# Performance work log

Measured on AMD Instinct MI355X. Metric: run time of the kernel, lower is better.

Reference implementation:

```python
import jax, jax.numpy as jnp
import numpy as np

N_NODES = 50000
N_EDGES = 800000
IN_DIM, HID_DIM, OUT_DIM, N_CLASSES = 128, 256, 64, 40


def _xavier(key, shape):
    fan_in, fan_out = shape[0], shape[1]
    std = float(np.sqrt(2.0 / (fan_in + fan_out)))
    return jax.random.normal(key, shape, dtype=jnp.float32) * std


def gcn_conv(x, W, b, src, dst, n_nodes):
    """PyG GCNConv: add self-loops, symmetric D^-1/2 (A+I) D^-1/2 X W + b."""
    h = x @ W  # [N, out]
    loop = jnp.arange(n_nodes, dtype=src.dtype)
    s = jnp.concatenate([src, loop])  # sources (messages flow src -> dst)
    d = jnp.concatenate([dst, loop])
    ones = jnp.ones(s.shape[0], dtype=h.dtype)
    deg = jax.ops.segment_sum(ones, d, num_segments=n_nodes)  # in-degree incl. self-loop
    dinv = jnp.where(deg > 0, jax.lax.rsqrt(deg), 0.0)
    norm = dinv[s] * dinv[d]  # [E+N]
    msg = h[s] * norm[:, None]
    out = jax.ops.segment_sum(msg, d, num_segments=n_nodes)
    return out + b


def setup_inputs() -> dict:
    key = jax.random.key(0)
    ks = jax.random.split(key, 9)
    x = jax.random.normal(ks[0], (N_NODES, IN_DIM), dtype=jnp.float32)
    edge_index = jax.random.randint(ks[1], (2, N_EDGES), 0, N_NODES, dtype=jnp.int64)
    return {
        "x": x,
        "edge_index": edge_index,
        "W1": _xavier(ks[2], (IN_DIM, HID_DIM)),
        "b1": jnp.zeros((HID_DIM,), jnp.float32),
        "W2": _xavier(ks[3], (HID_DIM, OUT_DIM)),
        "b2": jnp.zeros((OUT_DIM,), jnp.float32),
        "Wp1": _xavier(ks[4], (2 * OUT_DIM, 4 * OUT_DIM)),
        "bp1": jnp.zeros((4 * OUT_DIM,), jnp.float32),
        "Wp2": _xavier(ks[5], (4 * OUT_DIM, OUT_DIM)),
        "bp2": jnp.zeros((OUT_DIM,), jnp.float32),
        "Wc": _xavier(ks[6], (OUT_DIM, N_CLASSES)),
        "bc": jnp.zeros((N_CLASSES,), jnp.float32),
    }


def reference(x, edge_index, W1, b1, W2, b2, Wp1, bp1, Wp2, bp2, Wc, bc):
    src, dst = edge_index[0], edge_index[1]
    n = x.shape[0]
    h = jax.nn.relu(gcn_conv(x, W1, b1, src, dst, n))  # [N, HID]
    f = gcn_conv(h, W2, b2, src, dst, n)  # [N, OUT]
    # edge MLP on gathered endpoint features
    ef = jnp.concatenate([f[src], f[dst]], axis=-1)  # [E, 2*OUT]
    ef = jax.nn.relu(ef @ Wp1 + bp1)  # [E, 4*OUT]
    edge_feats = ef @ Wp2 + bp2  # [E, OUT]
    logits = f @ Wc + bc  # [N, C]
    return f, edge_feats, logits, edge_index
```

## Files before the change

### kernel.cpp

```cpp
#include <hip/hip_runtime.h>

#define N_NODES   50000
#define N_EDGES   800000
#define IN_DIM    128
#define HID_DIM   256
#define OUT_DIM   64
#define N_CLASSES 40

typedef __attribute__((ext_vector_type(8))) short short8;
typedef __attribute__((ext_vector_type(8))) unsigned short ushort8;
typedef __attribute__((ext_vector_type(4))) float f32x4;

__device__ inline short f2bf(float x) {
    unsigned u = __builtin_bit_cast(unsigned, x);
    unsigned r = (u + 0x7FFFu + ((u >> 16) & 1u)) >> 16;
    return (short)r;
}
__device__ inline float bf2f(unsigned short u) {
    unsigned v = ((unsigned)u) << 16;
    return __builtin_bit_cast(float, v);
}
__device__ __host__ inline int swap23(int p) {
    return (p & 0xC3) | ((p >> 2) & 0x0C) | ((p << 2) & 0x30);
}


__global__ void k_prep(const float* __restrict__ x,
                       const float* __restrict__ W1, const float* __restrict__ W2,
                       const float* __restrict__ Wp1, const float* __restrict__ Wp2,
                       unsigned short* __restrict__ xb,
                       short* __restrict__ W1t, short* __restrict__ W2t,
                       short* __restrict__ Wp1t, short* __restrict__ Wp2t,
                       int* __restrict__ degi, int* __restrict__ cursor) {
    int i = blockIdx.x * 256 + threadIdx.x;
    if (i < N_NODES) { degi[i] = 0; cursor[i] = 0; }
    if (i < 128 * 256) {
        int k = i >> 8, n = i & 255;
        W1t[n * 128 + k]  = f2bf(W1[i]);
        Wp1t[n * 128 + k] = f2bf(Wp1[i]);
    }
    if (i < 256 * 64) {
        int p = i >> 6, o = i & 63;
        int h = swap23(p);
        W2t[o * 256 + p]  = f2bf(W2[h * 64 + o]);
        Wp2t[o * 256 + p] = f2bf(Wp2[h * 64 + o]);
    }
    if (i < N_NODES * IN_DIM / 4) {
        float4 v = ((const float4*)x)[i];
        ushort4 u;
        u.x = (unsigned short)f2bf(v.x); u.y = (unsigned short)f2bf(v.y);
        u.z = (unsigned short)f2bf(v.z); u.w = (unsigned short)f2bf(v.w);
        ((ushort4*)xb)[i] = u;
    }
}


__global__ void k_deg_count(const int* __restrict__ dst, int* __restrict__ degi) {
    int e = blockIdx.x * 256 + threadIdx.x;
    if (e < N_EDGES) atomicAdd(&degi[dst[e]], 1);
}

__global__ void k_scan_bsum(const int* __restrict__ vals, int n, int* __restrict__ bsum,
                            float* __restrict__ dinv) {
    __shared__ int sm[256];
    int t = threadIdx.x, i = blockIdx.x * 256 + t;
    int d = (i < n) ? vals[i] : 0;
    if (i < n) dinv[i] = rsqrtf((float)(d + 1));
    sm[t] = d;
    __syncthreads();
    for (int s = 128; s > 0; s >>= 1) {
        if (t < s) sm[t] += sm[t + s];
        __syncthreads();
    }
    if (t == 0) bsum[blockIdx.x] = sm[0];
}

__global__ void k_scan_bscan(int* __restrict__ bsum, int nb) {
    __shared__ int sm[256];
    int t = threadIdx.x;
    int orig = (t < nb) ? bsum[t] : 0;
    sm[t] = orig;
    __syncthreads();
    for (int off = 1; off < 256; off <<= 1) {
        int v = (t >= off) ? sm[t - off] : 0;
        __syncthreads();
        sm[t] += v;
        __syncthreads();
    }
    if (t < nb) bsum[t] = sm[t] - orig;
}

__global__ void k_scan_final(const int* __restrict__ vals, int n,
                             const int* __restrict__ bscan, int* __restrict__ out) {
    __shared__ int sm[256];
    int t = threadIdx.x, i = blockIdx.x * 256 + t;
    int orig = (i < n) ? vals[i] : 0;
    sm[t] = orig;
    __syncthreads();
    for (int off = 1; off < 256; off <<= 1) {
        int v = (t >= off) ? sm[t - off] : 0;
        __syncthreads();
        sm[t] += v;
        __syncthreads();
    }
    int excl = sm[t] - orig + bscan[blockIdx.x];
    if (i < n) out[i] = excl;
    if (i == n - 1) out[n] = excl + orig;
}

__global__ void k_csr_fill(const int* __restrict__ src, const int* __restrict__ dst,
                           const int* __restrict__ csr_off, int* __restrict__ cursor,
                           int* __restrict__ csr_src) {
    int e = blockIdx.x * 256 + threadIdx.x;
    if (e < N_EDGES) {
        int d = dst[e];
        int pos = csr_off[d] + atomicAdd(&cursor[d], 1);
        csr_src[pos] = src[e];
    }
}

__global__ void k_copy_ei(const int* __restrict__ ei, float* __restrict__ out) {
    int j = blockIdx.x * 256 + threadIdx.x;
    if (j < (2 * N_EDGES) / 4) {
        int4 v = ((const int4*)ei)[j];
        float4 o = {(float)v.x, (float)v.y, (float)v.z, (float)v.w};
        ((float4*)out)[j] = o;
    }
}


__global__ __launch_bounds__(256) void k_agg0(const unsigned short* __restrict__ xb,
                                              const float* __restrict__ dinv,
                                              const int* __restrict__ csr_off,
                                              const int* __restrict__ csr_src,
                                              unsigned short* __restrict__ xa) {
    const int v = blockIdx.x * 4 + (threadIdx.x >> 6);
    const int lane = threadIdx.x & 63;
    float dv = dinv[v];
    unsigned c = *(const unsigned*)(xb + (size_t)v * 128 + lane * 2);
    float a0 = bf2f((unsigned short)(c & 0xFFFF)) * dv;
    float a1 = bf2f((unsigned short)(c >> 16)) * dv;
    int beg = csr_off[v], end = csr_off[v + 1];
    for (int base = beg; base < end; base += 64) {
        int idx = base + lane;
        int sj = (idx < end) ? csr_src[idx] : 0;
        float dj = (idx < end) ? dinv[sj] : 0.f;
        int m = min(64, end - base);
        int j = 0;
        for (; j + 4 <= m; j += 4) {
            int s0 = __shfl(sj, j), s1 = __shfl(sj, j + 1);
            int s2 = __shfl(sj, j + 2), s3 = __shfl(sj, j + 3);
            float d0 = __shfl(dj, j), d1 = __shfl(dj, j + 1);
            float d2 = __shfl(dj, j + 2), d3 = __shfl(dj, j + 3);
            unsigned h0 = *(const unsigned*)(xb + (size_t)s0 * 128 + lane * 2);
            unsigned h1 = *(const unsigned*)(xb + (size_t)s1 * 128 + lane * 2);
            unsigned h2 = *(const unsigned*)(xb + (size_t)s2 * 128 + lane * 2);
            unsigned h3 = *(const unsigned*)(xb + (size_t)s3 * 128 + lane * 2);
            a0 += bf2f((unsigned short)(h0 & 0xFFFF)) * d0 + bf2f((unsigned short)(h1 & 0xFFFF)) * d1
                + bf2f((unsigned short)(h2 & 0xFFFF)) * d2 + bf2f((unsigned short)(h3 & 0xFFFF)) * d3;
            a1 += bf2f((unsigned short)(h0 >> 16)) * d0 + bf2f((unsigned short)(h1 >> 16)) * d1
                + bf2f((unsigned short)(h2 >> 16)) * d2 + bf2f((unsigned short)(h3 >> 16)) * d3;
        }
        for (; j < m; j++) {
            int s = __shfl(sj, j);
            float ds = __shfl(dj, j);
            unsigned hv = *(const unsigned*)(xb + (size_t)s * 128 + lane * 2);
            a0 += bf2f((unsigned short)(hv & 0xFFFF)) * ds;
            a1 += bf2f((unsigned short)(hv >> 16)) * ds;
        }
    }
    unsigned o = (unsigned)(unsigned short)f2bf(a0 * dv) |
                 ((unsigned)(unsigned short)f2bf(a1 * dv) << 16);
    *(unsigned*)(xa + (size_t)v * 128 + lane * 2) = o;
}


__global__ __launch_bounds__(256) void k_agg2(const unsigned short* __restrict__ h2b,
                                              const float* __restrict__ dinv,
                                              const int* __restrict__ csr_off,
                                              const int* __restrict__ csr_src,
                                              const float* __restrict__ b2,
                                              const float* __restrict__ Wc,
                                              const float* __restrict__ bc,
                                              float* __restrict__ f_out,
                                              unsigned short* __restrict__ fb,
                                              float* __restrict__ lg_out) {
    const int v = blockIdx.x * 4 + (threadIdx.x >> 6);
    const int lane = threadIdx.x & 63;
    float dv = dinv[v];
    float acc = bf2f(h2b[(size_t)v * 64 + lane]) * dv;
    int beg = csr_off[v], end = csr_off[v + 1];
    for (int base = beg; base < end; base += 64) {
        int idx = base + lane;
        int sj = (idx < end) ? csr_src[idx] : 0;
        float dj = (idx < end) ? dinv[sj] : 0.f;
        int m = min(64, end - base);
        int j = 0;
        for (; j + 4 <= m; j += 4) {
            int s0 = __shfl(sj, j), s1 = __shfl(sj, j + 1);
            int s2 = __shfl(sj, j + 2), s3 = __shfl(sj, j + 3);
            float d0 = __shfl(dj, j), d1 = __shfl(dj, j + 1);
            float d2 = __shfl(dj, j + 2), d3 = __shfl(dj, j + 3);
            float h0 = bf2f(h2b[(size_t)s0 * 64 + lane]);
            float h1 = bf2f(h2b[(size_t)s1 * 64 + lane]);
            float h2 = bf2f(h2b[(size_t)s2 * 64 + lane]);
            float h3 = bf2f(h2b[(size_t)s3 * 64 + lane]);
            acc += h0 * d0 + h1 * d1 + h2 * d2 + h3 * d3;
        }
        for (; j < m; j++) {
            int s = __shfl(sj, j);
            float ds = __shfl(dj, j);
            acc += bf2f(h2b[(size_t)s * 64 + lane]) * ds;
        }
    }
    float r = acc * dv + b2[lane];
    f_out[(size_t)v * 64 + lane] = r;
    fb[(size_t)v * 64 + lane] = (unsigned short)f2bf(r);
    bool act = lane < N_CLASSES;
    float lacc = act ? bc[lane] : 0.f;
    #pragma unroll
    for (int i2 = 0; i2 < 64; i2++) {
        float fi = __shfl(r, i2);
        if (act) lacc += fi * Wc[i2 * N_CLASSES + lane];
    }
    if (act) lg_out[(size_t)v * N_CLASSES + lane] = lacc;
}


__global__ __launch_bounds__(256) void k_gemm1_mfma(const unsigned short* __restrict__ xa,
                                                    const short* __restrict__ W1t,
                                                    const float* __restrict__ b1,
                                                    unsigned short* __restrict__ h1) {
    __shared__ unsigned short xs[64 * 128];
    const int t = threadIdx.x;
    const int lane = t & 63, wv = t >> 6, lr = lane & 15, lg = lane >> 4;
    const int nb = blockIdx.x * 64;

    #pragma unroll
    for (int i = 0; i < 4; i++) {
        int q = t + i * 256, row = q >> 4, seg = q & 15;
        int node = nb + row;
        ushort8 v = {0, 0, 0, 0, 0, 0, 0, 0};
        if (node < N_NODES) v = *(const ushort8*)(xa + (size_t)node * 128 + seg * 8);
        *(ushort8*)((char*)xs + ((row * 256 + seg * 16) ^ ((row & 7) << 4))) = v;
    }

    short8 A1[4][4];
    #pragma unroll
    for (int mi = 0; mi < 4; mi++)
        #pragma unroll
        for (int kt = 0; kt < 4; kt++)
            A1[mi][kt] = *(const short8*)(W1t + (size_t)(wv * 64 + mi * 16 + lr) * 128 + kt * 32 + lg * 8);
    __syncthreads();

    #pragma unroll
    for (int nj = 0; nj < 4; nj++) {
        short8 Bf[4];
        int nr = nj * 16 + lr;
        #pragma unroll
        for (int kt = 0; kt < 4; kt++)
            Bf[kt] = *(const short8*)((const char*)xs + ((nr * 256 + kt * 64 + lg * 16) ^ ((nr & 7) << 4)));
        int node = nb + nr;
        #pragma unroll
        for (int mh = 0; mh < 2; mh++) {
            f32x4 a0 = {0.f, 0.f, 0.f, 0.f}, a1 = {0.f, 0.f, 0.f, 0.f};
            #pragma unroll
            for (int kt = 0; kt < 4; kt++) {
                a0 = __builtin_amdgcn_mfma_f32_16x16x32_bf16(A1[mh * 2 + 0][kt], Bf[kt], a0, 0, 0, 0);
                a1 = __builtin_amdgcn_mfma_f32_16x16x32_bf16(A1[mh * 2 + 1][kt], Bf[kt], a1, 0, 0, 0);
            }
            if (node < N_NODES) {
                float4 b0 = *(const float4*)(b1 + wv * 64 + (mh * 2 + 0) * 16 + lg * 4);
                float4 b1v = *(const float4*)(b1 + wv * 64 + (mh * 2 + 1) * 16 + lg * 4);
                ushort8 pk;
                pk[0] = (unsigned short)f2bf(fmaxf(a0[0] + b0.x, 0.f));
                pk[1] = (unsigned short)f2bf(fmaxf(a0[1] + b0.y, 0.f));
                pk[2] = (unsigned short)f2bf(fmaxf(a0[2] + b0.z, 0.f));
                pk[3] = (unsigned short)f2bf(fmaxf(a0[3] + b0.w, 0.f));
                pk[4] = (unsigned short)f2bf(fmaxf(a1[0] + b1v.x, 0.f));
                pk[5] = (unsigned short)f2bf(fmaxf(a1[1] + b1v.y, 0.f));
                pk[6] = (unsigned short)f2bf(fmaxf(a1[2] + b1v.z, 0.f));
                pk[7] = (unsigned short)f2bf(fmaxf(a1[3] + b1v.w, 0.f));
                *(ushort8*)(h1 + (size_t)node * 256 + wv * 64 + lg * 16 + mh * 8) = pk;
            }
        }
    }
}


__global__ __launch_bounds__(256) void k_gemm2_mfma(const unsigned short* __restrict__ h1,
                                                    const short* __restrict__ W2t,
                                                    unsigned short* __restrict__ h2b) {
    __shared__ unsigned short hs[64 * 256];
    const int t = threadIdx.x;
    const int lane = t & 63, wv = t >> 6, lr = lane & 15, lg = lane >> 4;
    const int nb = blockIdx.x * 64;

    #pragma unroll
    for (int i = 0; i < 8; i++) {
        int q = t + i * 256, row = q >> 5, seg = q & 31;
        int node = nb + row;
        ushort8 v = {0, 0, 0, 0, 0, 0, 0, 0};
        if (node < N_NODES) v = *(const ushort8*)(h1 + (size_t)node * 256 + seg * 8);
        *(ushort8*)((char*)hs + ((row * 512 + seg * 16) ^ ((row & 7) << 4))) = v;
    }

    short8 A2[8];
    #pragma unroll
    for (int kt = 0; kt < 8; kt++)
        A2[kt] = *(const short8*)(W2t + (size_t)(wv * 16 + lr) * 256 + kt * 32 + lg * 8);
    __syncthreads();

    #pragma unroll
    for (int nj = 0; nj < 4; nj++) {
        short8 Bh[8];
        int nr = nj * 16 + lr;
        #pragma unroll
        for (int kt = 0; kt < 8; kt++)
            Bh[kt] = *(const short8*)((const char*)hs + ((nr * 512 + kt * 64 + lg * 16) ^ ((nr & 7) << 4)));
        int node = nb + nr;
        f32x4 acc = {0.f, 0.f, 0.f, 0.f};
        #pragma unroll
        for (int kt = 0; kt < 8; kt++)
            acc = __builtin_amdgcn_mfma_f32_16x16x32_bf16(A2[kt], Bh[kt], acc, 0, 0, 0);
        if (node < N_NODES) {
            ushort4 u;
            u.x = (unsigned short)f2bf(acc[0]); u.y = (unsigned short)f2bf(acc[1]);
            u.z = (unsigned short)f2bf(acc[2]); u.w = (unsigned short)f2bf(acc[3]);
            *(ushort4*)(h2b + (size_t)node * 64 + wv * 16 + lg * 4) = u;
        }
    }
}


__global__ __launch_bounds__(256) void k_egather(const unsigned short* __restrict__ fb,
                                                 const int* __restrict__ src,
                                                 const int* __restrict__ dst,
                                                 char* __restrict__ ef_ws) {
    const int nchunk = N_EDGES * 16;
    for (int q = blockIdx.x * 256 + threadIdx.x; q < nchunk; q += gridDim.x * 256) {
        int e = q >> 4, seg = q & 15;
        int node = (seg < 8) ? src[e] : dst[e];
        ushort8 v = *(const ushort8*)(fb + (size_t)node * 64 + (seg & 7) * 8);
        *(ushort8*)(ef_ws + (size_t)e * 256 + seg * 16) = v;
    }
}


__global__ __launch_bounds__(256) void k_edge_mlpB(
        const char* __restrict__ ef_ws,
        const short* __restrict__ Wp1t, const float* __restrict__ bp1,
        const short* __restrict__ Wp2t, const float* __restrict__ bp2,
        float* __restrict__ out, int n_tiles) {
    __shared__ unsigned short hid_s[2][32 * 256];

    const int t = threadIdx.x;
    const int lane = t & 63, wv = t >> 6, lr = lane & 15, lg = lane >> 4;

    short8 A1[4][4];
    #pragma unroll
    for (int mi = 0; mi < 4; mi++)
        #pragma unroll
        for (int kt = 0; kt < 4; kt++)
            A1[mi][kt] = *(const short8*)(Wp1t + (size_t)(wv * 64 + mi * 16 + lr) * 128 + kt * 32 + lg * 8);
    float4 bb1[4];
    #pragma unroll
    for (int mi = 0; mi < 4; mi++)
        bb1[mi] = *(const float4*)(bp1 + wv * 64 + mi * 16 + lg * 4);
    const float4 bv2 = *(const float4*)(bp2 + wv * 16 + lg * 4);

    int tile = blockIdx.x;
    if (tile >= n_tiles) return;

    short8 Bf[2][4];
    {
        const char* base = ef_ws + (size_t)tile * 8192;
        #pragma unroll
        for (int nj = 0; nj < 2; nj++)
            #pragma unroll
            for (int kt = 0; kt < 4; kt++)
                Bf[nj][kt] = *(const short8*)(base + (nj * 16 + lr) * 256 + kt * 64 + lg * 16);
    }

    int cur = 0;
    for (; tile < n_tiles; tile += gridDim.x) {
        short8 A2[8];
        #pragma unroll
        for (int kt = 0; kt < 8; kt++)
            A2[kt] = *(const short8*)(Wp2t + (size_t)(wv * 16 + lr) * 256 + kt * 32 + lg * 8);

        #pragma unroll
        for (int nj = 0; nj < 2; nj++) {
            int er = nj * 16 + lr;
            #pragma unroll
            for (int mh = 0; mh < 2; mh++) {
                f32x4 a0 = {0.f, 0.f, 0.f, 0.f}, a1 = {0.f, 0.f, 0.f, 0.f};
                #pragma unroll
                for (int kt = 0; kt < 4; kt++) {
                    a0 = __builtin_amdgcn_mfma_f32_16x16x32_bf16(A1[mh * 2 + 0][kt], Bf[nj][kt], a0, 0, 0, 0);
                    a1 = __builtin_amdgcn_mfma_f32_16x16x32_bf16(A1[mh * 2 + 1][kt], Bf[nj][kt], a1, 0, 0, 0);
                }
                float4 b0 = bb1[mh * 2 + 0], b1v = bb1[mh * 2 + 1];
                ushort8 pk;
                pk[0] = (unsigned short)f2bf(fmaxf(a0[0] + b0.x, 0.f));
                pk[1] = (unsigned short)f2bf(fmaxf(a0[1] + b0.y, 0.f));
                pk[2] = (unsigned short)f2bf(fmaxf(a0[2] + b0.z, 0.f));
                pk[3] = (unsigned short)f2bf(fmaxf(a0[3] + b0.w, 0.f));
                pk[4] = (unsigned short)f2bf(fmaxf(a1[0] + b1v.x, 0.f));
                pk[5] = (unsigned short)f2bf(fmaxf(a1[1] + b1v.y, 0.f));
                pk[6] = (unsigned short)f2bf(fmaxf(a1[2] + b1v.z, 0.f));
                pk[7] = (unsigned short)f2bf(fmaxf(a1[3] + b1v.w, 0.f));
                *(ushort8*)((char*)hid_s[cur] +
                    ((er * 512 + wv * 128 + lg * 32 + mh * 16) ^ ((er & 7) << 4))) = pk;
            }
        }

        int tn = tile + gridDim.x;
        if (tn < n_tiles) {
            const char* nbase = ef_ws + (size_t)tn * 8192;
            #pragma unroll
            for (int nj = 0; nj < 2; nj++)
                #pragma unroll
                for (int kt = 0; kt < 4; kt++)
                    Bf[nj][kt] = *(const short8*)(nbase + (nj * 16 + lr) * 256 + kt * 64 + lg * 16);
        }

        asm volatile("s_waitcnt lgkmcnt(0)" ::: "memory");
        __builtin_amdgcn_s_barrier();

        #pragma unroll
        for (int nj = 0; nj < 2; nj++) {
            short8 Bh[8];
            int er = nj * 16 + lr;
            #pragma unroll
            for (int kt = 0; kt < 8; kt++)
                Bh[kt] = *(const short8*)((const char*)hid_s[cur] +
                             ((er * 512 + kt * 64 + lg * 16) ^ ((er & 7) << 4)));
            f32x4 acc = {0.f, 0.f, 0.f, 0.f};
            #pragma unroll
            for (int kt = 0; kt < 8; kt++)
                acc = __builtin_amdgcn_mfma_f32_16x16x32_bf16(A2[kt], Bh[kt], acc, 0, 0, 0);
            float4 o = {acc[0] + bv2.x, acc[1] + bv2.y, acc[2] + bv2.z, acc[3] + bv2.w};
            *(float4*)(out + (size_t)(tile * 32 + er) * 64 + wv * 16 + lg * 4) = o;
        }
        cur ^= 1;
    }
}


extern "C" void kernel_launch(void* const* d_in, const int* in_sizes, int n_in,
                              void* d_out, int out_size, void* d_ws, size_t ws_size,
                              hipStream_t stream) {
    const float* x   = (const float*)d_in[0];
    const int*   ei  = (const int*)d_in[1];
    const float* W1  = (const float*)d_in[2];
    const float* b1  = (const float*)d_in[3];
    const float* W2  = (const float*)d_in[4];
    const float* b2  = (const float*)d_in[5];
    const float* Wp1 = (const float*)d_in[6];
    const float* bp1 = (const float*)d_in[7];
    const float* Wp2 = (const float*)d_in[8];
    const float* bp2 = (const float*)d_in[9];
    const float* Wc  = (const float*)d_in[10];
    const float* bc  = (const float*)d_in[11];

    const int* src = ei;
    const int* dst = ei + N_EDGES;

    float* out    = (float*)d_out;
    float* f_out  = out;
    float* ef_out = out + (size_t)N_NODES * OUT_DIM;
    float* lg_out = ef_out + (size_t)N_EDGES * OUT_DIM;
    float* ei_out = lg_out + (size_t)N_NODES * N_CLASSES;

    char* p = (char*)d_ws;
    auto alloc = [&](size_t bytes) -> char* {
        char* r = p;
        p += (bytes + 255) / 256 * 256;
        return r;
    };
    char*           ef_ws = alloc((size_t)N_EDGES * 256);
    unsigned short* xb   = (unsigned short*)alloc((size_t)N_NODES * IN_DIM * 2);
    unsigned short* xa   = (unsigned short*)alloc((size_t)N_NODES * IN_DIM * 2);
    unsigned short* h1   = (unsigned short*)alloc((size_t)N_NODES * HID_DIM * 2);
    unsigned short* h2b  = (unsigned short*)alloc((size_t)N_NODES * OUT_DIM * 2);
    unsigned short* fb   = (unsigned short*)alloc((size_t)N_NODES * OUT_DIM * 2);
    int*   degi    = (int*)alloc((size_t)N_NODES * 4);
    float* dinv    = (float*)alloc((size_t)N_NODES * 4);
    int*   csr_off = (int*)alloc((size_t)(N_NODES + 1) * 4);
    int*   cursor  = (int*)alloc((size_t)N_NODES * 4);
    int*   csr_src = (int*)alloc((size_t)N_EDGES * 4);
    int*   bsum    = (int*)alloc(256 * 4);
    short* W1t     = (short*)alloc((size_t)256 * 128 * 2);
    short* W2t     = (short*)alloc((size_t)64 * 256 * 2);
    short* Wp1t    = (short*)alloc((size_t)256 * 128 * 2);
    short* Wp2t    = (short*)alloc((size_t)64 * 256 * 2);

    const int nbScan = (N_NODES + 255) / 256;

    k_prep<<<(N_NODES * IN_DIM / 4 + 255) / 256, 256, 0, stream>>>(
        x, W1, W2, Wp1, Wp2, xb, W1t, W2t, Wp1t, Wp2t, degi, cursor);
    k_deg_count<<<(N_EDGES + 255) / 256, 256, 0, stream>>>(dst, degi);
    k_scan_bsum<<<nbScan, 256, 0, stream>>>(degi, N_NODES, bsum, dinv);
    k_scan_bscan<<<1, 256, 0, stream>>>(bsum, nbScan);
    k_scan_final<<<nbScan, 256, 0, stream>>>(degi, N_NODES, bsum, csr_off);
    k_csr_fill<<<(N_EDGES + 255) / 256, 256, 0, stream>>>(src, dst, csr_off, cursor, csr_src);

    const int nbG = (N_NODES + 63) / 64;
    k_agg0<<<N_NODES / 4, 256, 0, stream>>>(xb, dinv, csr_off, csr_src, xa);
    k_gemm1_mfma<<<nbG, 256, 0, stream>>>(xa, W1t, b1, h1);
    k_gemm2_mfma<<<nbG, 256, 0, stream>>>(h1, W2t, h2b);
    k_agg2<<<N_NODES / 4, 256, 0, stream>>>(h2b, dinv, csr_off, csr_src, b2, Wc, bc,
                                            f_out, fb, lg_out);

    k_egather<<<2048, 256, 0, stream>>>(fb, src, dst, ef_ws);
    k_edge_mlpB<<<1024, 256, 0, stream>>>(ef_ws, Wp1t, bp1, Wp2t, bp2, ef_out, N_EDGES / 32);
    k_copy_ei<<<(2 * N_EDGES / 4 + 255) / 256, 256, 0, stream>>>(ei, ei_out);
}
```

Measured before the change: 464.6 us.

## Fuse endpoint gather into edge MLP kernel with prefetched edge indices

Removes the separate edge-gather kernel that materialized a 256-byte-per-edge bf16 buffer, and has the edge MLP kernel read src/dst rows of fb directly. Edge indices are prefetched two tiles ahead and feature rows one tile ahead to hide the indirect-load latency. The Wp2 fragment load is hoisted out of the tile loop, and the grid grows from 1024 to 1280 blocks. This saves roughly 400MB of workspace traffic but makes the MLP kernel's loads random-access with higher register pressure.

```diff
diff --git a/kernel.cpp b/kernel.cpp
--- a/kernel.cpp
+++ b/kernel.cpp
@@ -333,22 +333,9 @@
 }
 
 
-__global__ __launch_bounds__(256) void k_egather(const unsigned short* __restrict__ fb,
-                                                 const int* __restrict__ src,
-                                                 const int* __restrict__ dst,
-                                                 char* __restrict__ ef_ws) {
-    const int nchunk = N_EDGES * 16;
-    for (int q = blockIdx.x * 256 + threadIdx.x; q < nchunk; q += gridDim.x * 256) {
-        int e = q >> 4, seg = q & 15;
-        int node = (seg < 8) ? src[e] : dst[e];
-        ushort8 v = *(const ushort8*)(fb + (size_t)node * 64 + (seg & 7) * 8);
-        *(ushort8*)(ef_ws + (size_t)e * 256 + seg * 16) = v;
-    }
-}
-
-
-__global__ __launch_bounds__(256) void k_edge_mlpB(
-        const char* __restrict__ ef_ws,
+__global__ __launch_bounds__(256) void k_edge_mlpC(
+        const unsigned short* __restrict__ fb,
+        const int* __restrict__ src, const int* __restrict__ dst,
         const short* __restrict__ Wp1t, const float* __restrict__ bp1,
         const short* __restrict__ Wp2t, const float* __restrict__ bp2,
         float* __restrict__ out, int n_tiles) {
@@ -363,6 +350,10 @@
         #pragma unroll
         for (int kt = 0; kt < 4; kt++)
             A1[mi][kt] = *(const short8*)(Wp1t + (size_t)(wv * 64 + mi * 16 + lr) * 128 + kt * 32 + lg * 8);
+    short8 A2[8];
+    #pragma unroll
+    for (int kt = 0; kt < 8; kt++)
+        A2[kt] = *(const short8*)(Wp2t + (size_t)(wv * 16 + lr) * 256 + kt * 32 + lg * 8);
     float4 bb1[4];
     #pragma unroll
     for (int mi = 0; mi < 4; mi++)
@@ -371,24 +362,42 @@
 
     int tile = blockIdx.x;
     if (tile >= n_tiles) return;
+    const int g = gridDim.x;
 
     short8 Bf[2][4];
     {
-        const char* base = ef_ws + (size_t)tile * 8192;
-        #pragma unroll
-        for (int nj = 0; nj < 2; nj++)
-            #pragma unroll
-            for (int kt = 0; kt < 4; kt++)
-                Bf[nj][kt] = *(const short8*)(base + (nj * 16 + lr) * 256 + kt * 64 + lg * 16);
+        int sC[2], dC[2];
+        #pragma unroll
+        for (int nj = 0; nj < 2; nj++) {
+            int e = tile * 32 + nj * 16 + lr;
+            sC[nj] = src[e];
+            dC[nj] = dst[e];
+        }
+        #pragma unroll
+        for (int nj = 0; nj < 2; nj++) {
+            const unsigned short* srow = fb + (size_t)sC[nj] * 64;
+            const unsigned short* drow = fb + (size_t)dC[nj] * 64;
+            Bf[nj][0] = *(const short8*)(srow + lg * 8);
+            Bf[nj][1] = *(const short8*)(srow + 32 + lg * 8);
+            Bf[nj][2] = *(const short8*)(drow + lg * 8);
+            Bf[nj][3] = *(const short8*)(drow + 32 + lg * 8);
+        }
+    }
+    int sA[2], dA[2];
+    {
+        int tn = tile + g;
+        if (tn < n_tiles) {
+            #pragma unroll
+            for (int nj = 0; nj < 2; nj++) {
+                int e = tn * 32 + nj * 16 + lr;
+                sA[nj] = src[e];
+                dA[nj] = dst[e];
+            }
+        }
     }
 
     int cur = 0;
-    for (; tile < n_tiles; tile += gridDim.x) {
-        short8 A2[8];
-        #pragma unroll
-        for (int kt = 0; kt < 8; kt++)
-            A2[kt] = *(const short8*)(Wp2t + (size_t)(wv * 16 + lr) * 256 + kt * 32 + lg * 8);
-
+    for (; tile < n_tiles; tile += g) {
         #pragma unroll
         for (int nj = 0; nj < 2; nj++) {
             int er = nj * 16 + lr;
@@ -415,14 +424,26 @@
             }
         }
 
-        int tn = tile + gridDim.x;
+        int tn = tile + g;
         if (tn < n_tiles) {
-            const char* nbase = ef_ws + (size_t)tn * 8192;
-            #pragma unroll
-            for (int nj = 0; nj < 2; nj++)
-                #pragma unroll
-                for (int kt = 0; kt < 4; kt++)
-                    Bf[nj][kt] = *(const short8*)(nbase + (nj * 16 + lr) * 256 + kt * 64 + lg * 16);
+            #pragma unroll
+            for (int nj = 0; nj < 2; nj++) {
+                const unsigned short* srow = fb + (size_t)sA[nj] * 64;
+                const unsigned short* drow = fb + (size_t)dA[nj] * 64;
+                Bf[nj][0] = *(const short8*)(srow + lg * 8);
+                Bf[nj][1] = *(const short8*)(srow + 32 + lg * 8);
+                Bf[nj][2] = *(const short8*)(drow + lg * 8);
+                Bf[nj][3] = *(const short8*)(drow + 32 + lg * 8);
+            }
+        }
+        int tnn = tile + 2 * g;
+        if (tnn < n_tiles) {
+            #pragma unroll
+            for (int nj = 0; nj < 2; nj++) {
+                int e = tnn * 32 + nj * 16 + lr;
+                sA[nj] = src[e];
+                dA[nj] = dst[e];
+            }
         }
 
         asm volatile("s_waitcnt lgkmcnt(0)" ::: "memory");
@@ -479,7 +500,6 @@
         p += (bytes + 255) / 256 * 256;
         return r;
     };
-    char*           ef_ws = alloc((size_t)N_EDGES * 256);
     unsigned short* xb   = (unsigned short*)alloc((size_t)N_NODES * IN_DIM * 2);
     unsigned short* xa   = (unsigned short*)alloc((size_t)N_NODES * IN_DIM * 2);
     unsigned short* h1   = (unsigned short*)alloc((size_t)N_NODES * HID_DIM * 2);
@@ -513,7 +533,7 @@
     k_agg2<<<N_NODES / 4, 256, 0, stream>>>(h2b, dinv, csr_off, csr_src, b2, Wc, bc,
                                             f_out, fb, lg_out);
 
-    k_egather<<<2048, 256, 0, stream>>>(fb, src, dst, ef_ws);
-    k_edge_mlpB<<<1024, 256, 0, stream>>>(ef_ws, Wp1t, bp1, Wp2t, bp2, ef_out, N_EDGES / 32);
+    k_edge_mlpC<<<1280, 256, 0, stream>>>(fb, src, dst, Wp1t, bp1, Wp2t, bp2,
+                                          ef_out, N_EDGES / 32);
     k_copy_ei<<<(2 * N_EDGES / 4 + 255) / 256, 256, 0, stream>>>(ei, ei_out);
 }
```

Result: faster. 388.8 us (-16.3%).
